# Optimization experiments

Measured on AMD Instinct MI355X. Metric: run time of the kernel, lower is better.

Reference implementation:

```python
import jax, jax.numpy as jnp
import numpy as np

N_NODES = 50000
N_EDGES = 400000
NUM_FEATURES = 32
NUM_GRAPHS = 64
NUM_CLASSES = 2


def setup_inputs() -> dict:
    key = jax.random.key(0)
    ks = jax.random.split(key, 24)
    inp = {
        "x": jax.random.normal(ks[0], (N_NODES, NUM_FEATURES), dtype=jnp.float32),
        "edge_index": jax.random.randint(ks[1], (2, N_EDGES), 0, N_NODES),
        "edge_attr": jax.random.uniform(ks[2], (N_EDGES, 1), dtype=jnp.float32),
        "batch": jnp.sort(jax.random.randint(ks[3], (N_NODES,), 0, NUM_GRAPHS)),
        # nn1: Linear(1,10) -> ReLU -> Linear(10, 32*16)
        "nn1_w1": jax.random.normal(ks[4], (1, 10), dtype=jnp.float32) * 0.3,
        "nn1_b1": jnp.zeros((10,), jnp.float32),
        "nn1_w2": jax.random.normal(ks[5], (10, NUM_FEATURES * 16), dtype=jnp.float32) * 0.1,
        "nn1_b2": jnp.zeros((NUM_FEATURES * 16,), jnp.float32),
        "conv1_root": jax.random.normal(ks[6], (NUM_FEATURES, 16), dtype=jnp.float32) * 0.1,
        "conv1_bias": jnp.zeros((16,), jnp.float32),
        # nn2: Linear(1,10) -> ReLU -> Linear(10, 16*32)
        "nn2_w1": jax.random.normal(ks[7], (1, 10), dtype=jnp.float32) * 0.3,
        "nn2_b1": jnp.zeros((10,), jnp.float32),
        "nn2_w2": jax.random.normal(ks[8], (10, 16 * 32), dtype=jnp.float32) * 0.1,
        "nn2_b2": jnp.zeros((16 * 32,), jnp.float32),
        "conv2_root": jax.random.normal(ks[9], (16, 32), dtype=jnp.float32) * 0.15,
        "conv2_bias": jnp.zeros((32,), jnp.float32),
        "fc1_w": jax.random.normal(ks[10], (32, 64), dtype=jnp.float32) * 0.15,
        "fc1_b": jnp.zeros((64,), jnp.float32),
        "fc2_w": jax.random.normal(ks[11], (64, NUM_CLASSES), dtype=jnp.float32) * 0.1,
        "fc2_b": jnp.zeros((NUM_CLASSES,), jnp.float32),
    }
    return inp


def _nnconv(x, edge_src, edge_dst, edge_attr, w1, b1, w2, b2, root, bias, in_ch, out_ch):
    # Per-edge weight matrix from edge MLP: [E, in_ch, out_ch]
    h = jax.nn.relu(edge_attr @ w1 + b1) @ w2 + b2
    W = h.reshape(-1, in_ch, out_ch)
    msg = jnp.einsum('ei,eio->eo', x[edge_src], W)  # [E, out_ch]
    agg = jax.ops.segment_sum(msg, edge_dst, num_segments=N_NODES)
    cnt = jax.ops.segment_sum(jnp.ones((msg.shape[0],), x.dtype), edge_dst, num_segments=N_NODES)
    mean = agg / jnp.maximum(cnt, 1.0)[:, None]
    return mean + x @ root + bias


def reference(x, edge_index, edge_attr, batch,
              nn1_w1, nn1_b1, nn1_w2, nn1_b2, conv1_root, conv1_bias,
              nn2_w1, nn2_b1, nn2_w2, nn2_b2, conv2_root, conv2_bias,
              fc1_w, fc1_b, fc2_w, fc2_b):
    src, dst = edge_index[0], edge_index[1]
    h = jax.nn.elu(_nnconv(x, src, dst, edge_attr, nn1_w1, nn1_b1, nn1_w2, nn1_b2,
                           conv1_root, conv1_bias, NUM_FEATURES, 16))
    h = jax.nn.elu(_nnconv(h, src, dst, edge_attr, nn2_w1, nn2_b1, nn2_w2, nn2_b2,
                           conv2_root, conv2_bias, 16, 32))
    # global mean pool over graphs
    gsum = jax.ops.segment_sum(h, batch, num_segments=NUM_GRAPHS)
    gcnt = jax.ops.segment_sum(jnp.ones((h.shape[0],), h.dtype), batch, num_segments=NUM_GRAPHS)
    g = gsum / jnp.maximum(gcnt, 1.0)[:, None]
    g = jax.nn.elu(g @ fc1_w + fc1_b)
    return jax.nn.log_softmax(g @ fc2_w + fc2_b, axis=1)
```

## Files before the change

kernel.cpp:

```cpp
#include <hip/hip_runtime.h>
#include <hip/hip_fp16.h>
#include <math.h>

#define N_NODES 50000
#define N_EDGES 400000
#define NUM_GRAPHS 64


__global__ __launch_bounds__(256) void k1_p1(const float* __restrict__ x,
        const float* __restrict__ w2, const float* __restrict__ b2,
        const float* __restrict__ root, __half* __restrict__ P,
        float* __restrict__ R1) {
    __shared__ float Wl[32][192];
    __shared__ float xl[16][32];
    int t = threadIdx.x;
    for (int idx = t; idx < 32 * 192; idx += 256) {
        int i = idx / 192, c = idx % 192;
        int m = c >> 4, o = c & 15;
        float w;
        if (m < 10)       w = w2[m * 512 + i * 16 + o];
        else if (m == 10) w = b2[i * 16 + o];
        else              w = root[i * 16 + o];
        Wl[i][c] = w;
    }
    int n0 = blockIdx.x * 16;
    for (int idx = t; idx < 16 * 32; idx += 256) {
        int nl = idx >> 5, i = idx & 31;
        int n = n0 + nl;
        xl[nl][i] = (n < N_NODES) ? x[n * 32 + i] : 0.f;
    }
    __syncthreads();
    int nl = t >> 4, o = t & 15;
    int n = n0 + nl;
    if (n >= N_NODES) return;
    float acc[12];
#pragma unroll
    for (int m = 0; m < 12; m++) acc[m] = 0.f;
#pragma unroll
    for (int i = 0; i < 32; i++) {
        float xv = xl[nl][i];
#pragma unroll
        for (int m = 0; m < 12; m++) acc[m] += xv * Wl[i][m * 16 + o];
    }
    __half2* Po = (__half2*)(P + (size_t)n * 192 + o * 12);
#pragma unroll
    for (int k = 0; k < 6; k++) Po[k] = __floats2half2_rn(acc[2 * k], acc[2 * k + 1]);
    R1[n * 16 + o] = acc[11];
}

__global__ __launch_bounds__(256) void k4_p2(const float* __restrict__ agg1,
        const float* __restrict__ cnt, const float* __restrict__ R1,
        const float* __restrict__ bias1,
        const float* __restrict__ w2, const float* __restrict__ b2,
        const float* __restrict__ root, __half* __restrict__ P2,
        float* __restrict__ R2) {
    __shared__ float Wl[16][384];
    __shared__ float hl[8][16];
    int t = threadIdx.x;
    for (int idx = t; idx < 16 * 384; idx += 256) {
        int i = idx / 384, c = idx % 384;
        int m = c >> 5, o = c & 31;
        float w;
        if (m < 10)       w = w2[m * 512 + i * 32 + o];
        else if (m == 10) w = b2[i * 32 + o];
        else              w = root[i * 32 + o];
        Wl[i][c] = w;
    }
    int n0 = blockIdx.x * 8;
    if (t < 128) {
        int nl = t >> 4, i = t & 15;
        int n = n0 + nl;
        float v = 0.f;
        if (n < N_NODES) {
            float c = fmaxf(cnt[n], 1.0f);
            v = agg1[n * 16 + i] / c + R1[n * 16 + i] + bias1[i];
            v = v > 0.f ? v : expm1f(v);
        }
        hl[nl][i] = v;
    }
    __syncthreads();
    int nl = t >> 5, o = t & 31;
    int n = n0 + nl;
    if (n >= N_NODES) return;
    float acc[12];
#pragma unroll
    for (int m = 0; m < 12; m++) acc[m] = 0.f;
#pragma unroll
    for (int i = 0; i < 16; i++) {
        float hv = hl[nl][i];
#pragma unroll
        for (int m = 0; m < 12; m++) acc[m] += hv * Wl[i][m * 32 + o];
    }
    __half2* Po = (__half2*)(P2 + (size_t)n * 384 + o * 12);
#pragma unroll
    for (int k = 0; k < 6; k++) Po[k] = __floats2half2_rn(acc[2 * k], acc[2 * k + 1]);
    R2[(size_t)n * 32 + o] = acc[11];
}

__global__ __launch_bounds__(256) void k2_edge1(const __half* __restrict__ P,
        const int* __restrict__ src, const int* __restrict__ dst,
        const float* __restrict__ ea, const float* __restrict__ w1,
        const float* __restrict__ b1, float* __restrict__ agg,
        float* __restrict__ cnt) {
    int t = threadIdx.x;
    int e = blockIdx.x * 16 + (t >> 4);
    int o = t & 15;
    if (e >= N_EDGES) return;
    float a = ea[e];
    int s = src[e], d = dst[e];
    const float2* Pf = (const float2*)P;
    int base = s * 48 + o * 3;
    float2 f0 = Pf[base];
    float2 f1 = Pf[base + 1];
    float2 f2 = Pf[base + 2];
    float r[10];
#pragma unroll
    for (int j = 0; j < 10; j++) r[j] = fmaxf(a * w1[j] + b1[j], 0.f);
    union { float2 f; __half2 h[2]; } u;
    float m;
    {
        u.f = f2;
        float2 p89 = __half22float2(u.h[0]);
        float2 pQR = __half22float2(u.h[1]);
        m = pQR.x + r[8] * p89.x + r[9] * p89.y;
    }
    {
        u.f = f0;
        float2 p01 = __half22float2(u.h[0]);
        float2 p23 = __half22float2(u.h[1]);
        m += r[0] * p01.x + r[1] * p01.y + r[2] * p23.x + r[3] * p23.y;
    }
    {
        u.f = f1;
        float2 p45 = __half22float2(u.h[0]);
        float2 p67 = __half22float2(u.h[1]);
        m += r[4] * p45.x + r[5] * p45.y + r[6] * p67.x + r[7] * p67.y;
    }
    atomicAdd(agg + d * 16 + o, m);
    if (o == 0) atomicAdd(cnt + d, 1.0f);
}

__global__ __launch_bounds__(256) void k5_edge2(const __half* __restrict__ P,
        const int* __restrict__ src, const int* __restrict__ dst,
        const float* __restrict__ ea, const float* __restrict__ w1,
        const float* __restrict__ b1, float* __restrict__ agg) {
    int t = threadIdx.x;
    int e = blockIdx.x * 8 + (t >> 5);
    int o = t & 31;
    if (e >= N_EDGES) return;
    float a = ea[e];
    int s = src[e], d = dst[e];
    const float2* Pf = (const float2*)P;
    int base = s * 96 + o * 3;
    float2 f0 = Pf[base];
    float2 f1 = Pf[base + 1];
    float2 f2 = Pf[base + 2];
    float r[10];
#pragma unroll
    for (int j = 0; j < 10; j++) r[j] = fmaxf(a * w1[j] + b1[j], 0.f);
    union { float2 f; __half2 h[2]; } u;
    float m;
    {
        u.f = f2;
        float2 p89 = __half22float2(u.h[0]);
        float2 pQR = __half22float2(u.h[1]);
        m = pQR.x + r[8] * p89.x + r[9] * p89.y;
    }
    {
        u.f = f0;
        float2 p01 = __half22float2(u.h[0]);
        float2 p23 = __half22float2(u.h[1]);
        m += r[0] * p01.x + r[1] * p01.y + r[2] * p23.x + r[3] * p23.y;
    }
    {
        u.f = f1;
        float2 p45 = __half22float2(u.h[0]);
        float2 p67 = __half22float2(u.h[1]);
        m += r[4] * p45.x + r[5] * p45.y + r[6] * p67.x + r[7] * p67.y;
    }
    atomicAdd(agg + d * 32 + o, m);
}

__global__ __launch_bounds__(256) void k6_partial(const float* __restrict__ agg2,
        const float* __restrict__ cnt, const float* __restrict__ R2,
        const float* __restrict__ bias2, const int* __restrict__ batch,
        float* __restrict__ gsum) {
    const int NB = 512;
    const int chunk = (N_NODES + NB - 1) / NB;
    int begin = blockIdx.x * chunk;
    int end = begin + chunk;
    if (end > N_NODES) end = N_NODES;
    int t = threadIdx.x;
    int o = t & 31, ch = t >> 5;
    float bz = bias2[o];
    float acc = 0.f;
    int cur_g = -1;
    for (int n = begin + ch; n < end; n += 8) {
        int g = batch[n];
        float c = fmaxf(cnt[n], 1.0f);
        float v = agg2[(size_t)n * 32 + o] / c + R2[(size_t)n * 32 + o] + bz;
        v = v > 0.f ? v : expm1f(v);
        if (g != cur_g) {
            if (cur_g >= 0) atomicAdd(gsum + cur_g * 32 + o, acc);
            cur_g = g; acc = 0.f;
        }
        acc += v;
    }
    if (cur_g >= 0) atomicAdd(gsum + cur_g * 32 + o, acc);
}

__global__ __launch_bounds__(256) void k8_head(const float* __restrict__ gsum,
        const int* __restrict__ batch,
        const float* __restrict__ fc1w, const float* __restrict__ fc1b,
        const float* __restrict__ fc2w, const float* __restrict__ fc2b,
        float* __restrict__ out) {
    __shared__ float gl[64][32];
    __shared__ float w1l[32][64];
    __shared__ float hl[64][64];
    __shared__ float zl[64][2];
    __shared__ float gc[64];
    int t = threadIdx.x;
    if (t < 64) {
        int g = t;
        int lo = 0, hi = N_NODES;
        while (lo < hi) { int mid = (lo + hi) >> 1; if (batch[mid] < g) lo = mid + 1; else hi = mid; }
        int s0 = lo;
        lo = 0; hi = N_NODES;
        while (lo < hi) { int mid = (lo + hi) >> 1; if (batch[mid] < g + 1) lo = mid + 1; else hi = mid; }
        gc[g] = fmaxf((float)(lo - s0), 1.0f);
    }
    for (int idx = t; idx < 32 * 64; idx += 256) w1l[idx >> 6][idx & 63] = fc1w[idx];
    __syncthreads();
    for (int idx = t; idx < 64 * 32; idx += 256) gl[idx >> 5][idx & 31] = gsum[idx] / gc[idx >> 5];
    __syncthreads();
    for (int idx = t; idx < 64 * 64; idx += 256) {
        int gg = idx >> 6, c = idx & 63;
        float acc = fc1b[c];
#pragma unroll
        for (int i = 0; i < 32; i++) acc += gl[gg][i] * w1l[i][c];
        hl[gg][c] = acc > 0.f ? acc : expm1f(acc);
    }
    __syncthreads();
    if (t < 128) {
        int gg = t >> 1, k = t & 1;
        float acc = fc2b[k];
#pragma unroll
        for (int c = 0; c < 64; c++) acc += hl[gg][c] * fc2w[c * 2 + k];
        zl[gg][k] = acc;
    }
    __syncthreads();
    if (t < 128) {
        int gg = t >> 1, k = t & 1;
        float z0 = zl[gg][0], z1 = zl[gg][1];
        float m = fmaxf(z0, z1);
        float lse = m + logf(expf(z0 - m) + expf(z1 - m));
        out[t] = zl[gg][k] - lse;
    }
}

extern "C" void kernel_launch(void* const* d_in, const int* in_sizes, int n_in,
                              void* d_out, int out_size, void* d_ws, size_t ws_size,
                              hipStream_t stream) {
    const float* x       = (const float*)d_in[0];
    const int*   ei      = (const int*)d_in[1];
    const float* ea      = (const float*)d_in[2];
    const int*   batch   = (const int*)d_in[3];
    const float* nn1_w1  = (const float*)d_in[4];
    const float* nn1_b1  = (const float*)d_in[5];
    const float* nn1_w2  = (const float*)d_in[6];
    const float* nn1_b2  = (const float*)d_in[7];
    const float* c1_root = (const float*)d_in[8];
    const float* c1_bias = (const float*)d_in[9];
    const float* nn2_w1  = (const float*)d_in[10];
    const float* nn2_b1  = (const float*)d_in[11];
    const float* nn2_w2  = (const float*)d_in[12];
    const float* nn2_b2  = (const float*)d_in[13];
    const float* c2_root = (const float*)d_in[14];
    const float* c2_bias = (const float*)d_in[15];
    const float* fc1w    = (const float*)d_in[16];
    const float* fc1b    = (const float*)d_in[17];
    const float* fc2w    = (const float*)d_in[18];
    const float* fc2b    = (const float*)d_in[19];
    const int* src = ei;
    const int* dst = ei + N_EDGES;

    char* ws = (char*)d_ws;
    __half* P1 = (__half*)ws;
    __half* P2 = (__half*)(ws + (size_t)N_NODES * 192 * 2);
    float* fbase = (float*)(ws + (size_t)N_NODES * 192 * 2 + (size_t)N_NODES * 384 * 2);
    float* cnt  = fbase;
    float* agg1 = cnt + N_NODES;
    float* agg2 = agg1 + (size_t)N_NODES * 16;
    float* gsum = agg2 + (size_t)N_NODES * 32;
    float* R1   = gsum + NUM_GRAPHS * 32;
    float* R2   = R1 + (size_t)N_NODES * 16;

    hipMemsetAsync(cnt, 0,
        (size_t)(N_NODES + N_NODES * 16 + N_NODES * 32 + NUM_GRAPHS * 32) * sizeof(float), stream);

    k1_p1<<<(N_NODES + 15) / 16, 256, 0, stream>>>(x, nn1_w2, nn1_b2, c1_root, P1, R1);
    k2_edge1<<<(N_EDGES + 15) / 16, 256, 0, stream>>>(P1, src, dst, ea, nn1_w1, nn1_b1, agg1, cnt);
    k4_p2<<<(N_NODES + 7) / 8, 256, 0, stream>>>(agg1, cnt, R1, c1_bias, nn2_w2, nn2_b2, c2_root, P2, R2);
    k5_edge2<<<(N_EDGES + 7) / 8, 256, 0, stream>>>(P2, src, dst, ea, nn2_w1, nn2_b1, agg2);
    k6_partial<<<512, 256, 0, stream>>>(agg2, cnt, R2, c2_bias, batch, gsum);
    k8_head<<<1, 256, 0, stream>>>(gsum, batch, fc1w, fc1b, fc2w, fc2b, (float*)d_out);
}
```

Baseline: 281.8 us.

## Counting-sort edges by source so edge kernels gather P rows with locality

```diff
diff --git a/kernel.cpp b/kernel.cpp
--- a/kernel.cpp
+++ b/kernel.cpp
@@ -6,6 +6,55 @@
 #define N_EDGES 400000
 #define NUM_GRAPHS 64
 
+
+__global__ __launch_bounds__(256) void k0_hist(const int* __restrict__ src,
+        const int* __restrict__ dst, int* __restrict__ deg, int* __restrict__ cntd) {
+    int e = blockIdx.x * 256 + threadIdx.x;
+    if (e < N_EDGES) {
+        atomicAdd(deg + src[e], 1);
+        atomicAdd(cntd + dst[e], 1);
+    }
+}
+
+__global__ __launch_bounds__(1024) void k0_scan(const int* __restrict__ deg,
+        int* __restrict__ woff) {
+    __shared__ int part[1024];
+    int t = threadIdx.x;
+    const int C = (N_NODES + 1023) / 1024;
+    int base = t * C;
+    int s = 0;
+    for (int i = 0; i < C; i++) {
+        int n = base + i;
+        if (n < N_NODES) s += deg[n];
+    }
+    part[t] = s;
+    __syncthreads();
+    for (int off = 1; off < 1024; off <<= 1) {
+        int v = (t >= off) ? part[t - off] : 0;
+        __syncthreads();
+        part[t] += v;
+        __syncthreads();
+    }
+    int run = (t == 0) ? 0 : part[t - 1];
+    for (int i = 0; i < C; i++) {
+        int n = base + i;
+        if (n < N_NODES) { woff[n] = run; run += deg[n]; }
+    }
+}
+
+__global__ __launch_bounds__(256) void k0_scatter(const int* __restrict__ src,
+        const int* __restrict__ dst, const float* __restrict__ ea,
+        int* __restrict__ woff, int* __restrict__ ses, int* __restrict__ sed,
+        float* __restrict__ sea) {
+    int e = blockIdx.x * 256 + threadIdx.x;
+    if (e < N_EDGES) {
+        int s = src[e];
+        int pos = atomicAdd(woff + s, 1);
+        ses[pos] = s;
+        sed[pos] = dst[e];
+        sea[pos] = ea[e];
+    }
+}
 
 __global__ __launch_bounds__(256) void k1_p1(const float* __restrict__ x,
         const float* __restrict__ w2, const float* __restrict__ b2,
@@ -49,7 +98,7 @@
 }
 
 __global__ __launch_bounds__(256) void k4_p2(const float* __restrict__ agg1,
-        const float* __restrict__ cnt, const float* __restrict__ R1,
+        const int* __restrict__ cntd, const float* __restrict__ R1,
         const float* __restrict__ bias1,
         const float* __restrict__ w2, const float* __restrict__ b2,
         const float* __restrict__ root, __half* __restrict__ P2,
@@ -72,7 +121,8 @@
         int n = n0 + nl;
         float v = 0.f;
         if (n < N_NODES) {
-            float c = fmaxf(cnt[n], 1.0f);
+            int ci = cntd[n];
+            float c = (float)(ci > 0 ? ci : 1);
             v = agg1[n * 16 + i] / c + R1[n * 16 + i] + bias1[i];
             v = v > 0.f ? v : expm1f(v);
         }
@@ -98,16 +148,15 @@
 }
 
 __global__ __launch_bounds__(256) void k2_edge1(const __half* __restrict__ P,
-        const int* __restrict__ src, const int* __restrict__ dst,
-        const float* __restrict__ ea, const float* __restrict__ w1,
-        const float* __restrict__ b1, float* __restrict__ agg,
-        float* __restrict__ cnt) {
+        const int* __restrict__ ses, const int* __restrict__ sed,
+        const float* __restrict__ sea, const float* __restrict__ w1,
+        const float* __restrict__ b1, float* __restrict__ agg) {
     int t = threadIdx.x;
     int e = blockIdx.x * 16 + (t >> 4);
     int o = t & 15;
     if (e >= N_EDGES) return;
-    float a = ea[e];
-    int s = src[e], d = dst[e];
+    float a = sea[e];
+    int s = ses[e], d = sed[e];
     const float2* Pf = (const float2*)P;
     int base = s * 48 + o * 3;
     float2 f0 = Pf[base];
@@ -137,19 +186,18 @@
         m += r[4] * p45.x + r[5] * p45.y + r[6] * p67.x + r[7] * p67.y;
     }
     atomicAdd(agg + d * 16 + o, m);
-    if (o == 0) atomicAdd(cnt + d, 1.0f);
 }
 
 __global__ __launch_bounds__(256) void k5_edge2(const __half* __restrict__ P,
-        const int* __restrict__ src, const int* __restrict__ dst,
-        const float* __restrict__ ea, const float* __restrict__ w1,
+        const int* __restrict__ ses, const int* __restrict__ sed,
+        const float* __restrict__ sea, const float* __restrict__ w1,
         const float* __restrict__ b1, float* __restrict__ agg) {
     int t = threadIdx.x;
     int e = blockIdx.x * 8 + (t >> 5);
     int o = t & 31;
     if (e >= N_EDGES) return;
-    float a = ea[e];
-    int s = src[e], d = dst[e];
+    float a = sea[e];
+    int s = ses[e], d = sed[e];
     const float2* Pf = (const float2*)P;
     int base = s * 96 + o * 3;
     float2 f0 = Pf[base];
@@ -182,7 +230,7 @@
 }
 
 __global__ __launch_bounds__(256) void k6_partial(const float* __restrict__ agg2,
-        const float* __restrict__ cnt, const float* __restrict__ R2,
+        const int* __restrict__ cntd, const float* __restrict__ R2,
         const float* __restrict__ bias2, const int* __restrict__ batch,
         float* __restrict__ gsum) {
     const int NB = 512;
@@ -197,7 +245,8 @@
     int cur_g = -1;
     for (int n = begin + ch; n < end; n += 8) {
         int g = batch[n];
-        float c = fmaxf(cnt[n], 1.0f);
+        int ci = cntd[n];
+        float c = (float)(ci > 0 ? ci : 1);
         float v = agg2[(size_t)n * 32 + o] / c + R2[(size_t)n * 32 + o] + bz;
         v = v > 0.f ? v : expm1f(v);
         if (g != cur_g) {
@@ -285,23 +334,32 @@
     const int* dst = ei + N_EDGES;
 
     char* ws = (char*)d_ws;
-    __half* P1 = (__half*)ws;
-    __half* P2 = (__half*)(ws + (size_t)N_NODES * 192 * 2);
-    float* fbase = (float*)(ws + (size_t)N_NODES * 192 * 2 + (size_t)N_NODES * 384 * 2);
-    float* cnt  = fbase;
-    float* agg1 = cnt + N_NODES;
-    float* agg2 = agg1 + (size_t)N_NODES * 16;
-    float* gsum = agg2 + (size_t)N_NODES * 32;
-    float* R1   = gsum + NUM_GRAPHS * 32;
-    float* R2   = R1 + (size_t)N_NODES * 16;
-
-    hipMemsetAsync(cnt, 0,
-        (size_t)(N_NODES + N_NODES * 16 + N_NODES * 32 + NUM_GRAPHS * 32) * sizeof(float), stream);
-
+    size_t off = 0;
+    __half* P1 = (__half*)(ws + off); off += (size_t)N_NODES * 192 * 2;
+    __half* P2 = (__half*)(ws + off); off += (size_t)N_NODES * 384 * 2;
+    float* R1  = (float*)(ws + off);  off += (size_t)N_NODES * 16 * 4;
+    float* R2  = (float*)(ws + off);  off += (size_t)N_NODES * 32 * 4;
+    char* zbase = ws + off;
+    int*   deg  = (int*)(ws + off);   off += (size_t)N_NODES * 4;
+    int*   cntd = (int*)(ws + off);   off += (size_t)N_NODES * 4;
+    float* agg1 = (float*)(ws + off); off += (size_t)N_NODES * 16 * 4;
+    float* agg2 = (float*)(ws + off); off += (size_t)N_NODES * 32 * 4;
+    float* gsum = (float*)(ws + off); off += (size_t)NUM_GRAPHS * 32 * 4;
+    size_t zbytes = (size_t)(ws + off - zbase);
+    int*   woff = (int*)(ws + off);   off += (size_t)N_NODES * 4;
+    int*   ses  = (int*)(ws + off);   off += (size_t)N_EDGES * 4;
+    int*   sed  = (int*)(ws + off);   off += (size_t)N_EDGES * 4;
+    float* sea  = (float*)(ws + off); off += (size_t)N_EDGES * 4;
+
+    hipMemsetAsync(zbase, 0, zbytes, stream);
+
+    k0_hist<<<(N_EDGES + 255) / 256, 256, 0, stream>>>(src, dst, deg, cntd);
+    k0_scan<<<1, 1024, 0, stream>>>(deg, woff);
+    k0_scatter<<<(N_EDGES + 255) / 256, 256, 0, stream>>>(src, dst, ea, woff, ses, sed, sea);
     k1_p1<<<(N_NODES + 15) / 16, 256, 0, stream>>>(x, nn1_w2, nn1_b2, c1_root, P1, R1);
-    k2_edge1<<<(N_EDGES + 15) / 16, 256, 0, stream>>>(P1, src, dst, ea, nn1_w1, nn1_b1, agg1, cnt);
-    k4_p2<<<(N_NODES + 7) / 8, 256, 0, stream>>>(agg1, cnt, R1, c1_bias, nn2_w2, nn2_b2, c2_root, P2, R2);
-    k5_edge2<<<(N_EDGES + 7) / 8, 256, 0, stream>>>(P2, src, dst, ea, nn2_w1, nn2_b1, agg2);
-    k6_partial<<<512, 256, 0, stream>>>(agg2, cnt, R2, c2_bias, batch, gsum);
+    k2_edge1<<<(N_EDGES + 15) / 16, 256, 0, stream>>>(P1, ses, sed, sea, nn1_w1, nn1_b1, agg1);
+    k4_p2<<<(N_NODES + 7) / 8, 256, 0, stream>>>(agg1, cntd, R1, c1_bias, nn2_w2, nn2_b2, c2_root, P2, R2);
+    k5_edge2<<<(N_EDGES + 7) / 8, 256, 0, stream>>>(P2, ses, sed, sea, nn2_w1, nn2_b1, agg2);
+    k6_partial<<<512, 256, 0, stream>>>(agg2, cntd, R2, c2_bias, batch, gsum);
     k8_head<<<1, 256, 0, stream>>>(gsum, batch, fc1w, fc1b, fc2w, fc2b, (float*)d_out);
 }
```

Result: slower. 407.8 us (+44.7%).
